# Kernel tuning notes

Hardware: AMD Instinct MI355X
Metric: run time of the kernel (lower is better)

The kernel has to match this reference:

```python
import jax, jax.numpy as jnp
import numpy as np

# ResNet-20 (CIFAR) conv shapes: conv1 + 18 block convs, all 3x3 pad=1
SHAPES = [(16,3,3,3)] + [(16,16,3,3)]*6 + [(32,16,3,3)] + [(32,32,3,3)]*5 + [(64,32,3,3)] + [(64,64,3,3)]*5
SIZES = [int(np.prod(s)) for s in SHAPES]
OFFS = np.concatenate([[0], np.cumsum(SIZES)]).astype(int)
D = int(OFFS[-1])  # 267696 flattened conv params
LOW_D = 40
# (conv_a, conv_b, stride, out_channels) for each BasicBlock
BLOCKS = [(1,2,1,16),(3,4,1,16),(5,6,1,16),
          (7,8,2,32),(9,10,1,32),(11,12,1,32),
          (13,14,2,64),(15,16,1,64),(17,18,1,64)]

def conv3x3(x, w, stride):
    return jax.lax.conv_general_dilated(x, w, (stride, stride), ((1,1),(1,1)),
        dimension_numbers=('NCHW','OIHW','NCHW'))

def bn(x):
    # training-mode BatchNorm2d with default-initialized affine (gamma=1, beta=0)
    m = jnp.mean(x, axis=(0,2,3), keepdims=True)
    v = jnp.var(x, axis=(0,2,3), keepdims=True)
    return (x - m) * jax.lax.rsqrt(v + 1e-5)

def shortcut(x, stride, out_ch):
    # option-A shortcut: stride-2 subsample + zero-pad channels
    if stride != 1:
        x = x[:, :, ::2, ::2]
    pad = out_ch - x.shape[1]
    if pad > 0:
        x = jnp.pad(x, ((0,0),(pad//2, pad - pad//2),(0,0),(0,0)))
    return x

def setup_inputs() -> dict:
    key = jax.random.key(0)
    ks = jax.random.split(key, 6)
    B = 1024
    x = jax.random.normal(ks[0], (B,3,32,32), jnp.float32)
    origin_weight = jax.random.normal(ks[1], (D,), jnp.float32) * 0.05
    P = jax.random.normal(ks[2], (LOW_D, D), jnp.float32) * 0.01
    new_param = jax.random.uniform(ks[3], (LOW_D,), jnp.float32)
    W_fc = jax.random.normal(ks[4], (10,64), jnp.float32) * 0.1
    b_fc = jnp.zeros((10,), jnp.float32)
    return {"x": x, "origin_weight": origin_weight, "P": P,
            "new_param": new_param, "W_fc": W_fc, "b_fc": b_fc}

def reference(x, origin_weight, P, new_param, W_fc, b_fc):
    # conv(x, W0) + sum_i a_i * conv(x, P_i)  ==  conv(x, W0 + sum_i a_i * P_i)
    # (conv is linear in its weights, so fusing the 40-term loop is exact)
    w_flat = origin_weight + new_param @ P  # [D]
    ws = [w_flat[OFFS[i]:OFFS[i+1]].reshape(SHAPES[i]) for i in range(19)]
    out = jax.nn.relu(bn(conv3x3(x, ws[0], 1)))
    for (a, b, s, c) in BLOCKS:
        h = jax.nn.relu(bn(conv3x3(out, ws[a], s)))
        h = bn(conv3x3(h, ws[b], 1))
        out = jax.nn.relu(h + shortcut(out, s, c))
    out = out.mean(axis=(2,3))  # global average pool -> [B, 64]
    return out @ W_fc.T + b_fc  # [B, 10]
```

## Files before the change

kernel.cpp:

```cpp
#include <hip/hip_runtime.h>
#include <hip/hip_bf16.h>

#define BATCH 1024
#define NLAYER 19
#define DTOT 267696
#define NSLOT 64
#define PSL (NSLOT*128)

typedef __attribute__((ext_vector_type(8))) short v8s;
typedef __attribute__((ext_vector_type(4))) float v4f;

__device__ inline float ldf(const float* p){ return *p; }
__device__ inline float ldf(const __hip_bfloat16* p){ return __bfloat162float(*p); }

__device__ inline unsigned short f2bf(float x){
    __hip_bfloat16 h = __float2bfloat16(x);
    return *reinterpret_cast<unsigned short*>(&h);
}
__device__ inline float bf2f(unsigned int u){
    return __uint_as_float(u << 16);
}

__global__ void detect_kernel(const unsigned short* __restrict__ xraw, int* __restrict__ flag)
{
    __shared__ int bad;
    if (threadIdx.x == 0) bad = 0;
    __syncthreads();
    int lbad = 0;
    for (int i = threadIdx.x; i < 4096; i += 256) {
        unsigned e = (xraw[i] >> 7) & 0xFF;
        if (e >= 147) lbad++;
    }
    if (lbad) atomicAdd(&bad, lbad);
    __syncthreads();
    if (threadIdx.x == 0) *flag = (bad == 0) ? 1 : 0;
}

__device__ inline bool is_bf16(const int* flag)
{
    return (*(volatile const int*)flag) == 1;
}

__global__ void wflat_kernel(const void* __restrict__ origin,
                             const void* __restrict__ P,
                             const void* __restrict__ npar,
                             float* __restrict__ wout, int D,
                             const int* flag)
{
    int d = blockIdx.x*256 + threadIdx.x;
    if (d >= D) return;
    float acc;
    if (is_bf16(flag)) {
        const __hip_bfloat16* ob = (const __hip_bfloat16*)origin;
        const __hip_bfloat16* Pb = (const __hip_bfloat16*)P;
        const __hip_bfloat16* nb = (const __hip_bfloat16*)npar;
        acc = ldf(ob + d);
        #pragma unroll 8
        for (int k = 0; k < 40; k++)
            acc += ldf(nb + k) * ldf(Pb + (long long)k*D + d);
    } else {
        const float* of = (const float*)origin;
        const float* Pf = (const float*)P;
        const float* nf = (const float*)npar;
        acc = of[d];
        #pragma unroll 8
        for (int k = 0; k < 40; k++)
            acc += nf[k] * Pf[(long long)k*D + d];
    }
    wout[d] = acc;
}

__global__ void wprep_kernel(const float* __restrict__ wflat, unsigned short* __restrict__ WT)
{
    static const int CINA[19]  = {3,16,16,16,16,16,16,16,32,32,32,32,32,32,64,64,64,64,64};
    static const int COUTA[19] = {16,16,16,16,16,16,16,32,32,32,32,32,32,64,64,64,64,64,64};
    static const int LGCA[19]  = {0,4,4,4,4,4,4,4,5,5,5,5,5,5,6,6,6,6,6};
    static const int KPADA[19] = {0,160,160,160,160,160,160,160,288,288,288,288,288,288,576,576,576,576,576};
    static const int WOFFA[19] = {0,432,2736,5040,7344,9648,11952,14256,18864,
        28080,37296,46512,55728,64944,83376,120240,157104,193968,230832};
    static const int WTOFFA[19]= {0,0,2560,5120,7680,10240,12800,15360,20480,29696,
        38912,48128,57344,66560,84992,121856,158720,195584,232448};
    int l = blockIdx.z;
    if (l == 0) return;
    int co = blockIdx.y;
    if (co >= COUTA[l]) return;
    int kp = blockIdx.x*192 + threadIdx.x;
    if (kp >= KPADA[l]) return;
    int cin = CINA[l];
    float v = 0.f;
    if (kp < 9*cin) {
        int tap = kp >> LGCA[l];
        int ci  = kp & (cin - 1);
        v = wflat[WOFFA[l] + (co*cin + ci)*9 + tap];
    }
    WT[WTOFFA[l] + co*KPADA[l] + kp] = f2bf(v);
}

__device__ inline void ldpair_f(const float* base, int p, float& x0, float& x1){
    const float2 v = ((const float2*)base)[p];
    x0 = v.x; x1 = v.y;
}
__device__ inline void ldpair_h(const __hip_bfloat16* base, int p, float& x0, float& x1){
    unsigned u = ((const unsigned int*)base)[p];
    x0 = __uint_as_float(u << 16);
    x1 = __uint_as_float(u & 0xffff0000u);
}

__global__ __launch_bounds__(512) void conv_l0(
    const void* __restrict__ in, const float* __restrict__ wt,
    unsigned short* __restrict__ out, float* __restrict__ ps,
    const int* flag)
{
    constexpr int WP = 38, W2 = 19;
    __shared__ uint2 smem2[2048];
    __shared__ unsigned int in_su[3*18*W2];
    __shared__ float sred[8][32];

    const int tid  = threadIdx.x;
    const int b    = blockIdx.x >> 1;
    const int half = blockIdx.x & 1;
    const int row0 = half*16 - 1;
    const bool isbf = is_bf16(flag);

    {
        const __hip_bfloat16* inb_h = (const __hip_bfloat16*)in + (size_t)b*3072;
        const float*          inb_f = (const float*)in + (size_t)b*3072;
        for (int i = tid; i < 864; i += 512) {
            int w2 = i & 15, lr = (i >> 4) % 18, c = i / 288;
            int ih = row0 + lr;
            unsigned int pk = 0u;
            if ((unsigned)ih < 32u) {
                float x0, x1;
                if (isbf) ldpair_h(inb_h, (c*32 + ih)*16 + w2, x0, x1);
                else      ldpair_f(inb_f, (c*32 + ih)*16 + w2, x0, x1);
                pk = (unsigned int)f2bf(x0) | ((unsigned int)f2bf(x1) << 16);
            }
            in_su[(c*18 + lr)*W2 + 1 + w2] = pk;
        }
        unsigned short* in_ss = (unsigned short*)in_su;
        for (int i = tid; i < 54; i += 512) {
            in_ss[i*WP + 1]  = 0;
            in_ss[i*WP + 34] = 0;
        }
    }
    __syncthreads();

    const int r   = tid >> 5;
    const int col = tid & 31;
    const bool odd = (col & 1);

    float xin[27];
    #pragma unroll
    for (int ci = 0; ci < 3; ci++) {
        #pragma unroll
        for (int kh = 0; kh < 3; kh++) {
            const unsigned int* up = in_su + (ci*18 + r + kh)*W2 + ((col+1) >> 1);
            unsigned int u0 = up[0], u1 = up[1];
            const int kb = ci*9 + kh*3;
            xin[kb+0] = odd ? bf2f(u0 & 0xffffu) : bf2f(u0 >> 16);
            xin[kb+1] = odd ? bf2f(u0 >> 16)     : bf2f(u1 & 0xffffu);
            xin[kb+2] = odd ? bf2f(u1 & 0xffffu) : bf2f(u1 >> 16);
        }
    }

    float acc[16];
    #pragma unroll
    for (int co = 0; co < 16; co++) {
        float a = 0.f;
        #pragma unroll
        for (int k = 0; k < 27; k++)
            a += xin[k] * wt[co*27 + k];
        acc[co] = a;
    }

    #pragma unroll
    for (int j = 0; j < 4; j++) {
        uint2 v;
        v.x = (unsigned)f2bf(acc[4*j+0]) | ((unsigned)f2bf(acc[4*j+1]) << 16);
        v.y = (unsigned)f2bf(acc[4*j+2]) | ((unsigned)f2bf(acc[4*j+3]) << 16);
        smem2[tid*4 + (j ^ (tid & 3))] = v;
    }
    __syncthreads();

    float s4[4] = {0,0,0,0}, q4[4] = {0,0,0,0};
    {
        uint2* ob = (uint2*)(out + (size_t)b*16384 + half*8192);
        #pragma unroll
        for (int it = 0; it < 4; it++) {
            int s = it*512 + tid;
            int phys = (s & ~3) | ((s & 3) ^ ((s >> 2) & 3));
            uint2 v = smem2[phys];
            ob[s] = v;
            float f0 = bf2f(v.x & 0xffffu), f1v = bf2f(v.x >> 16);
            float f2v = bf2f(v.y & 0xffffu), f3v = bf2f(v.y >> 16);
            s4[0] += f0;  q4[0] += f0*f0;
            s4[1] += f1v; q4[1] += f1v*f1v;
            s4[2] += f2v; q4[2] += f2v*f2v;
            s4[3] += f3v; q4[3] += f3v*f3v;
        }
    }
    #pragma unroll
    for (int off = 4; off < 64; off <<= 1) {
        #pragma unroll
        for (int k2 = 0; k2 < 4; k2++) {
            s4[k2] += __shfl_xor(s4[k2], off);
            q4[k2] += __shfl_xor(q4[k2], off);
        }
    }
    {
        const int lane = tid & 63, wv = tid >> 6;
        if (lane < 4) {
            #pragma unroll
            for (int k2 = 0; k2 < 4; k2++) {
                sred[wv][lane*4 + k2]      = s4[k2];
                sred[wv][16 + lane*4 + k2] = q4[k2];
            }
        }
    }
    __syncthreads();
    if (tid < 32) {
        float a = 0.f;
        #pragma unroll
        for (int wv = 0; wv < 8; wv++) a += sred[wv][tid];
        float* sl = ps + (blockIdx.x & (NSLOT-1))*128;
        atomicAdd(&sl[(tid < 16) ? tid : (48 + tid)], a);
    }
}

template<int CIN, int COUT, int HIN, int WIN, int ST, bool FUSE, bool PN,
         bool FUSE2, int PREVC, int PADF>
__global__ __launch_bounds__(256, 4) void conv_mfma(
    const unsigned short* __restrict__ src, const unsigned short* __restrict__ prev,
    unsigned short* __restrict__ resid,
    const unsigned short* __restrict__ wt,
    unsigned short* __restrict__ out, float* __restrict__ stats,
    const float* __restrict__ nstats, float ninvN,
    const float* __restrict__ pstats, float pinvN)
{
    constexpr int HO = HIN/ST, WO = WIN/ST, M = HO*WO, MT = M/16;
    constexpr int NT = COUT/16;
    constexpr int K  = 9*CIN;
    constexpr int S  = (K + 31)/32;
    constexpr int KPAD = S*32;
    constexpr int lgC  = (CIN==16)?4:(CIN==32)?5:6;
    constexpr int lgWI = (WIN==32)?5:(WIN==16)?4:3;
    constexpr int lgWO = (WO==32)?5:(WO==16)?4:3;
    constexpr int CMASK = CIN/8 - 1;
    constexpr int JITER = (NT==1)? MT/4 : (NT==2)? MT/2 : MT;
    static_assert(M*COUT <= CIN*HIN*WIN, "out_s fits in in_s");

    __shared__ unsigned short in_s[CIN*HIN*WIN];
    __shared__ float red[128];
    __shared__ float statred[256];
    __shared__ float nm[64], nv[64];
    __shared__ float pm_s[64], pv_s[64];
    __shared__ uint4 zq;

    const int tid = threadIdx.x;
    const int b   = blockIdx.x;

    if (tid == 0) { zq.x = 0; zq.y = 0; zq.z = 0; zq.w = 0; }

    {
        const int idx = tid & 127, hf = tid >> 7;
        float sacc = 0.f;
        #pragma unroll 8
        for (int k = hf*32; k < hf*32 + 32; k++)
            sacc += nstats[k*128 + idx];
        statred[tid] = sacc;
    }
    __syncthreads();
    if (tid < CIN) {
        float ssum = statred[tid]      + statred[128 + tid];
        float qsum = statred[64 + tid] + statred[192 + tid];
        float m = ssum*ninvN;
        float v = fmaxf(qsum*ninvN - m*m, 0.f);
        nm[tid] = m; nv[tid] = rsqrtf(v + 1e-5f);
    }
    if (PN && tid < CIN) {
        float ssum = 0.f, qsum = 0.f;
        for (int k = 0; k < NSLOT; k++) {
            ssum += pstats[k*128 + tid];
            qsum += pstats[k*128 + 64 + tid];
        }
        float m = ssum*pinvN;
        float v = fmaxf(qsum*pinvN - m*m, 0.f);
        pm_s[tid] = m; pv_s[tid] = rsqrtf(v + 1e-5f);
    }
    __syncthreads();

    {
        const uint4* sb4 = (const uint4*)(src + (size_t)b*(HIN*WIN)*CIN);
        constexpr int NP4 = CIN*HIN*WIN/8;
        if (FUSE) {
            const uint4* pb4 = (const uint4*)(prev + (size_t)b*(HIN*WIN)*CIN);
            uint4* rb4 = (uint4*)(resid + (size_t)b*(HIN*WIN)*CIN);
            for (int i = tid; i < NP4; i += 256) {
                uint4 v = sb4[i];
                uint4 pw = pb4[i];
                int e0 = i << 3;
                int c0 = e0 & (CIN-1);
                int p  = e0 >> lgC;
                float f[8] = { bf2f(v.x & 0xffffu), bf2f(v.x >> 16),
                               bf2f(v.y & 0xffffu), bf2f(v.y >> 16),
                               bf2f(v.z & 0xffffu), bf2f(v.z >> 16),
                               bf2f(v.w & 0xffffu), bf2f(v.w >> 16) };
                float g[8] = { bf2f(pw.x & 0xffffu), bf2f(pw.x >> 16),
                               bf2f(pw.y & 0xffffu), bf2f(pw.y >> 16),
                               bf2f(pw.z & 0xffffu), bf2f(pw.z >> 16),
                               bf2f(pw.w & 0xffffu), bf2f(pw.w >> 16) };
                #pragma unroll
                for (int k = 0; k < 8; k++) {
                    int c = c0 + k;
                    float fx = (f[k] - nm[c])*nv[c];
                    float gv = g[k];
                    if (PN) gv = fmaxf((gv - pm_s[c])*pv_s[c], 0.f);
                    f[k] = fmaxf(fx + gv, 0.f);
                }
                uint4 o;
                o.x = (unsigned)f2bf(f[0]) | ((unsigned)f2bf(f[1]) << 16);
                o.y = (unsigned)f2bf(f[2]) | ((unsigned)f2bf(f[3]) << 16);
                o.z = (unsigned)f2bf(f[4]) | ((unsigned)f2bf(f[5]) << 16);
                o.w = (unsigned)f2bf(f[6]) | ((unsigned)f2bf(f[7]) << 16);
                rb4[i] = o;
                int csw = c0 ^ ((p & CMASK) << 3);
                *(uint4*)(in_s + (p << lgC) + csw) = o;
            }
        } else if (FUSE2) {
            uint4* rb4 = (uint4*)(resid + (size_t)b*(HIN*WIN)*CIN);
            for (int i = tid; i < NP4; i += 256) {
                uint4 v = sb4[i];
                int e0 = i << 3;
                int c0 = e0 & (CIN-1);
                int p  = e0 >> lgC;
                int h  = p >> lgWI, wq = p & (WIN-1);
                int pp = (h << (lgWI+2)) + 2*wq;
                int pc0 = c0 - PADF;
                bool pv = (pc0 >= 0) && (pc0 <= PREVC - 8);
                uint4 pw;
                pw.x = 0; pw.y = 0; pw.z = 0; pw.w = 0;
                if (pv) pw = *(const uint4*)(prev + ((size_t)b*(HIN*WIN*4) + pp)*PREVC + pc0);
                float f[8] = { bf2f(v.x & 0xffffu), bf2f(v.x >> 16),
                               bf2f(v.y & 0xffffu), bf2f(v.y >> 16),
                               bf2f(v.z & 0xffffu), bf2f(v.z >> 16),
                               bf2f(v.w & 0xffffu), bf2f(v.w >> 16) };
                float g[8] = { bf2f(pw.x & 0xffffu), bf2f(pw.x >> 16),
                               bf2f(pw.y & 0xffffu), bf2f(pw.y >> 16),
                               bf2f(pw.z & 0xffffu), bf2f(pw.z >> 16),
                               bf2f(pw.w & 0xffffu), bf2f(pw.w >> 16) };
                #pragma unroll
                for (int k = 0; k < 8; k++) {
                    int c = c0 + k;
                    f[k] = fmaxf((f[k] - nm[c])*nv[c] + g[k], 0.f);
                }
                uint4 o;
                o.x = (unsigned)f2bf(f[0]) | ((unsigned)f2bf(f[1]) << 16);
                o.y = (unsigned)f2bf(f[2]) | ((unsigned)f2bf(f[3]) << 16);
                o.z = (unsigned)f2bf(f[4]) | ((unsigned)f2bf(f[5]) << 16);
                o.w = (unsigned)f2bf(f[6]) | ((unsigned)f2bf(f[7]) << 16);
                rb4[i] = o;
                int csw = c0 ^ ((p & CMASK) << 3);
                *(uint4*)(in_s + (p << lgC) + csw) = o;
            }
        } else {
            for (int i = tid; i < NP4; i += 256) {
                uint4 v = sb4[i];
                int e0 = i << 3;
                int c0 = e0 & (CIN-1);
                int p  = e0 >> lgC;
                float f[8] = { bf2f(v.x & 0xffffu), bf2f(v.x >> 16),
                               bf2f(v.y & 0xffffu), bf2f(v.y >> 16),
                               bf2f(v.z & 0xffffu), bf2f(v.z >> 16),
                               bf2f(v.w & 0xffffu), bf2f(v.w >> 16) };
                #pragma unroll
                for (int k = 0; k < 8; k++) {
                    int c = c0 + k;
                    f[k] = fmaxf((f[k] - nm[c])*nv[c], 0.f);
                }
                uint4 o;
                o.x = (unsigned)f2bf(f[0]) | ((unsigned)f2bf(f[1]) << 16);
                o.y = (unsigned)f2bf(f[2]) | ((unsigned)f2bf(f[3]) << 16);
                o.z = (unsigned)f2bf(f[4]) | ((unsigned)f2bf(f[5]) << 16);
                o.w = (unsigned)f2bf(f[6]) | ((unsigned)f2bf(f[7]) << 16);
                int csw = c0 ^ ((p & CMASK) << 3);
                *(uint4*)(in_s + (p << lgC) + csw) = o;
            }
        }
    }
    __syncthreads();

    const int w   = tid >> 6;
    const int ln  = tid & 63;
    const int l15 = ln & 15;
    const int q   = ln >> 4;

    int n0, mt0, step;
    if (NT == 1)      { n0 = 0;         mt0 = w;      step = 4; }
    else if (NT == 2) { n0 = (w&1)*16;  mt0 = w>>1;   step = 2; }
    else              { n0 = w*16;      mt0 = 0;      step = 1; }

    const unsigned short* wb = wt + (size_t)(n0 + l15)*KPAD + q*8;
    const int c0q = (CIN==16) ? ((q & 1) << 3) : (q << 3);

    v4f acc[JITER];
    #pragma unroll
    for (int j = 0; j < JITER; j++) acc[j] = v4f{0.f,0.f,0.f,0.f};

    if constexpr (CIN == 64) {
        #pragma unroll
        for (int s = 0; s < S; s++) {
            const v8s Bf = *(const v8s*)(wb + 32*s);
            const int tap = s >> 1;
            const int dh1 = tap/3 - 1, dw1 = tap%3 - 1;
            const int c0s = c0q + ((s & 1) << 5);
            #pragma unroll
            for (int j = 0; j < JITER; j++) {
                const int mt  = mt0 + j*step;
                const int p   = mt*16 + l15;
                const int ihb = (p >> lgWO) * ST;
                const int iwb = (p & (WO-1)) * ST;
                int ih = ihb + dh1, iw = iwb + dw1;
                bool valid = ((unsigned)ih < (unsigned)HIN) && ((unsigned)iw < (unsigned)WIN);
                int pp  = (ih << lgWI) + iw;
                int csw = c0s ^ ((pp & CMASK) << 3);
                int eoff = (pp << lgC) + csw;
                const v8s* ap = valid ? (const v8s*)(in_s + eoff) : (const v8s*)&zq;
                v8s Af = *ap;
                acc[j] = __builtin_amdgcn_mfma_f32_16x16x32_bf16(Af, Bf, acc[j], 0, 0, 0);
            }
        }
    } else {
        v8s Bf[S];
        #pragma unroll
        for (int s = 0; s < S; s++)
            Bf[s] = *(const v8s*)(wb + 32*s);

        int dh1s[S], dw1s[S];
        if (CIN == 16) {
            int tq = q >> 1;
            #pragma unroll
            for (int s = 0; s < S; s++) {
                int tap = 2*s + tq;
                int dh = (tap*11) >> 5;
                int dw = tap - 3*dh;
                dh1s[s] = (tap >= 9) ? -1000 : (dh - 1);
                dw1s[s] = dw - 1;
            }
        }

        #pragma unroll
        for (int j = 0; j < JITER; j++) {
            const int mt  = mt0 + j*step;
            const int p   = mt*16 + l15;
            const int ihb = (p >> lgWO) * ST;
            const int iwb = (p & (WO-1)) * ST;
            #pragma unroll
            for (int s = 0; s < S; s++) {
                int dh1, dw1;
                if (CIN == 16) { dh1 = dh1s[s]; dw1 = dw1s[s]; }
                else           { dh1 = s/3 - 1; dw1 = s%3 - 1; }
                int ih = ihb + dh1, iw = iwb + dw1;
                bool valid = ((unsigned)ih < (unsigned)HIN) && ((unsigned)iw < (unsigned)WIN);
                int pp  = (ih << lgWI) + iw;
                int csw = c0q ^ ((pp & CMASK) << 3);
                int eoff = (pp << lgC) + csw;
                const v8s* ap = valid ? (const v8s*)(in_s + eoff) : (const v8s*)&zq;
                v8s Af = *ap;
                acc[j] = __builtin_amdgcn_mfma_f32_16x16x32_bf16(Af, Bf[s], acc[j], 0, 0, 0);
            }
        }
    }
    __syncthreads();

    unsigned short* out_s = in_s;
    float sa = 0.f, qa = 0.f;
    #pragma unroll
    for (int j = 0; j < JITER; j++) {
        const int mt = mt0 + j*step;
        #pragma unroll
        for (int r2 = 0; r2 < 4; r2++) {
            float v = acc[j][r2];
            out_s[(mt*16 + q*4 + r2)*COUT + n0 + l15] = f2bf(v);
            sa += v; qa += v*v;
        }
    }
    __syncthreads();

    {
        constexpr int NIT = (M*COUT/8)/256;
        uint4* ob4 = (uint4*)(out + (size_t)b*M*COUT);
        const uint4* os4 = (const uint4*)in_s;
        #pragma unroll
        for (int it = 0; it < NIT; it++)
            ob4[it*256 + tid] = os4[it*256 + tid];
    }

    sa += __shfl_xor(sa, 16); sa += __shfl_xor(sa, 32);
    qa += __shfl_xor(qa, 16); qa += __shfl_xor(qa, 32);
    if (q == 0) {
        red[(w*16 + l15)*2]     = sa;
        red[(w*16 + l15)*2 + 1] = qa;
    }
    __syncthreads();
    if (tid < COUT) {
        float S2, Q2;
        if (NT == 1) {
            S2 = red[tid*2] + red[(16+tid)*2] + red[(32+tid)*2] + red[(48+tid)*2];
            Q2 = red[tid*2+1] + red[(16+tid)*2+1] + red[(32+tid)*2+1] + red[(48+tid)*2+1];
        } else if (NT == 2) {
            int w0 = tid >> 4, cl = tid & 15;
            S2 = red[((w0*16)+cl)*2]     + red[(((w0+2)*16)+cl)*2];
            Q2 = red[((w0*16)+cl)*2 + 1] + red[(((w0+2)*16)+cl)*2 + 1];
        } else {
            int w0 = tid >> 4, cl = tid & 15;
            S2 = red[((w0*16)+cl)*2];
            Q2 = red[((w0*16)+cl)*2 + 1];
        }
        float* sl = stats + (b & (NSLOT-1))*128;
        atomicAdd(&sl[tid],      S2);
        atomicAdd(&sl[64 + tid], Q2);
    }
}

__global__ void poolfc_kernel(const unsigned short* __restrict__ x,
    const unsigned short* __restrict__ resid,
    const float* __restrict__ stats, float invN,
    const void* __restrict__ Wfc, const void* __restrict__ bfc,
    void* __restrict__ out, const int* flag)
{
    int b = blockIdx.x;
    int c = threadIdx.x;
    float ssum = 0.f, qsum = 0.f;
    for (int k = 0; k < NSLOT; k++) {
        ssum += stats[k*128 + c];
        qsum += stats[k*128 + 64 + c];
    }
    float m = ssum*invN;
    float v = fmaxf(qsum*invN - m*m, 0.f);
    float rs = rsqrtf(v + 1e-5f);
    float s = 0.f;
    #pragma unroll
    for (int p = 0; p < 64; p++) {
        size_t idx = ((size_t)b*64 + p)*64 + c;
        float xv = bf2f((unsigned int)x[idx]);
        float rv = bf2f((unsigned int)resid[idx]);
        s += fmaxf((xv - m)*rs + rv, 0.f);
    }
    __shared__ float feat[64];
    feat[c] = s * (1.f/64.f);
    __syncthreads();
    if (c < 10) {
        if (is_bf16(flag)) {
            const __hip_bfloat16* W  = (const __hip_bfloat16*)Wfc;
            const __hip_bfloat16* bb = (const __hip_bfloat16*)bfc;
            float o = ldf(bb + c);
            for (int k = 0; k < 64; k++)
                o += feat[k] * ldf(W + c*64 + k);
            ((__hip_bfloat16*)out)[b*10 + c] = __float2bfloat16(o);
        } else {
            const float* W  = (const float*)Wfc;
            const float* bb = (const float*)bfc;
            float o = bb[c];
            for (int k = 0; k < 64; k++)
                o += feat[k] * W[c*64 + k];
            ((float*)out)[b*10 + c] = o;
        }
    }
}

extern "C" void kernel_launch(void* const* d_in, const int* in_sizes, int n_in,
                              void* d_out, int out_size, void* d_ws, size_t ws_size,
                              hipStream_t stream)
{
    char* ws = (char*)d_ws;
    float* wflat = (float*)(ws);
    int*   flag  = (int*)  (ws + 1146880);
    unsigned short* WT = (unsigned short*)(ws + 1179648);
    unsigned short* curA = (unsigned short*)(ws + 1720320);
    unsigned short* curB = (unsigned short*)(ws + 1720320 + 33554432ULL);
    unsigned short* f1   = (unsigned short*)(ws + 1720320 + 67108864ULL);
    unsigned short* f2   = (unsigned short*)(ws + 1720320 + 100663296ULL);
    float* ps    = (float*)(ws + 135938048ULL);

    hipMemsetAsync(ps, 0, NLAYER*PSL*4, stream);
    detect_kernel<<<1, 256, 0, stream>>>((const unsigned short*)d_in[0], flag);

    wflat_kernel<<<(DTOT+255)/256, 256, 0, stream>>>(
        d_in[1], d_in[2], d_in[3], wflat, DTOT, flag);

    {
        dim3 g(3, 64, 19);
        wprep_kernel<<<g, 192, 0, stream>>>(wflat, WT);
    }

    static const int WTOFF[NLAYER] = {0,0,2560,5120,7680,10240,12800,15360,20480,29696,
        38912,48128,57344,66560,84992,121856,158720,195584,232448};
    const float iN32 = 1.f/1048576.f;
    const float iN16 = 1.f/262144.f;
    const float iN8  = 1.f/65536.f;

    conv_l0<<<2*BATCH,512,0,stream>>>(d_in[0], wflat, curB, ps, flag);

    conv_mfma<16,16,32,32,1,false,false,false,0,0><<<BATCH,256,0,stream>>>(
        curB, nullptr, nullptr, WT + WTOFF[1], f1, ps + 1*PSL, ps, iN32, nullptr, 0.f);
    conv_mfma<16,16,32,32,1,false,false,false,0,0><<<BATCH,256,0,stream>>>(
        f1, nullptr, nullptr, WT + WTOFF[2], f2, ps + 2*PSL, ps + 1*PSL, iN32, nullptr, 0.f);
    conv_mfma<16,16,32,32,1,true,true,false,0,0><<<BATCH,256,0,stream>>>(
        f2, curB, curA, WT + WTOFF[3], f1, ps + 3*PSL, ps + 2*PSL, iN32, ps, iN32);
    conv_mfma<16,16,32,32,1,false,false,false,0,0><<<BATCH,256,0,stream>>>(
        f1, nullptr, nullptr, WT + WTOFF[4], f2, ps + 4*PSL, ps + 3*PSL, iN32, nullptr, 0.f);
    conv_mfma<16,16,32,32,1,true,false,false,0,0><<<BATCH,256,0,stream>>>(
        f2, curA, curB, WT + WTOFF[5], f1, ps + 5*PSL, ps + 4*PSL, iN32, nullptr, 0.f);
    conv_mfma<16,16,32,32,1,false,false,false,0,0><<<BATCH,256,0,stream>>>(
        f1, nullptr, nullptr, WT + WTOFF[6], f2, ps + 6*PSL, ps + 5*PSL, iN32, nullptr, 0.f);
    conv_mfma<16,32,32,32,2,true,false,false,0,0><<<BATCH,256,0,stream>>>(
        f2, curB, curA, WT + WTOFF[7], f1, ps + 7*PSL, ps + 6*PSL, iN32, nullptr, 0.f);
    conv_mfma<32,32,16,16,1,false,false,false,0,0><<<BATCH,256,0,stream>>>(
        f1, nullptr, nullptr, WT + WTOFF[8], f2, ps + 8*PSL, ps + 7*PSL, iN16, nullptr, 0.f);
    conv_mfma<32,32,16,16,1,false,false,true,16,8><<<BATCH,256,0,stream>>>(
        f2, curA, curB, WT + WTOFF[9], f1, ps + 9*PSL, ps + 8*PSL, iN16, nullptr, 0.f);
    conv_mfma<32,32,16,16,1,false,false,false,0,0><<<BATCH,256,0,stream>>>(
        f1, nullptr, nullptr, WT + WTOFF[10], f2, ps + 10*PSL, ps + 9*PSL, iN16, nullptr, 0.f);
    conv_mfma<32,32,16,16,1,true,false,false,0,0><<<BATCH,256,0,stream>>>(
        f2, curB, curA, WT + WTOFF[11], f1, ps + 11*PSL, ps + 10*PSL, iN16, nullptr, 0.f);
    conv_mfma<32,32,16,16,1,false,false,false,0,0><<<BATCH,256,0,stream>>>(
        f1, nullptr, nullptr, WT + WTOFF[12], f2, ps + 12*PSL, ps + 11*PSL, iN16, nullptr, 0.f);
    conv_mfma<32,64,16,16,2,true,false,false,0,0><<<BATCH,256,0,stream>>>(
        f2, curA, curB, WT + WTOFF[13], f1, ps + 13*PSL, ps + 12*PSL, iN16, nullptr, 0.f);
    conv_mfma<64,64,8,8,1,false,false,false,0,0><<<BATCH,256,0,stream>>>(
        f1, nullptr, nullptr, WT + WTOFF[14], f2, ps + 14*PSL, ps + 13*PSL, iN8, nullptr, 0.f);
    conv_mfma<64,64,8,8,1,false,false,true,32,16><<<BATCH,256,0,stream>>>(
        f2, curB, curA, WT + WTOFF[15], f1, ps + 15*PSL, ps + 14*PSL, iN8, nullptr, 0.f);
    conv_mfma<64,64,8,8,1,false,false,false,0,0><<<BATCH,256,0,stream>>>(
        f1, nullptr, nullptr, WT + WTOFF[16], f2, ps + 16*PSL, ps + 15*PSL, iN8, nullptr, 0.f);
    conv_mfma<64,64,8,8,1,true,false,false,0,0><<<BATCH,256,0,stream>>>(
        f2, curA, curB, WT + WTOFF[17], f1, ps + 17*PSL, ps + 16*PSL, iN8, nullptr, 0.f);
    conv_mfma<64,64,8,8,1,false,false,false,0,0><<<BATCH,256,0,stream>>>(
        f1, nullptr, nullptr, WT + WTOFF[18], f2, ps + 18*PSL, ps + 17*PSL, iN8, nullptr, 0.f);

    poolfc_kernel<<<BATCH, 64, 0, stream>>>(
        f2, curB, ps + 18*PSL, iN8, d_in[4], d_in[5], d_out, flag);
}
```

Measured before the change: 459.2 us.

## Rewrite first conv layer as MFMA bf16 matmul with one image per block

The 3-channel first convolution drops its per-thread scalar FMA loop over 27 taps × 16 channels. It becomes an im2col-style bf16 MFMA (16x16x32) with K padded from 27 to 32, and each block now handles a whole image using 256 threads instead of half an image with 512. The input is staged into a zero-padded LDS tile and outputs are written back through LDS as 16-byte stores. BN statistics are computed from the fp32 accumulators rather than the bf16-rounded values, which slightly changes the numerics. Weights are also rounded to bf16, a possible accuracy change.

Measured after the change: 436.6 us. 4.9% less time.

```diff
diff --git a/kernel.cpp b/kernel.cpp
--- a/kernel.cpp
+++ b/kernel.cpp
@@ -96,134 +96,116 @@
     WT[WTOFFA[l] + co*KPADA[l] + kp] = f2bf(v);
 }
 
-__device__ inline void ldpair_f(const float* base, int p, float& x0, float& x1){
-    const float2 v = ((const float2*)base)[p];
-    x0 = v.x; x1 = v.y;
-}
-__device__ inline void ldpair_h(const __hip_bfloat16* base, int p, float& x0, float& x1){
-    unsigned u = ((const unsigned int*)base)[p];
-    x0 = __uint_as_float(u << 16);
-    x1 = __uint_as_float(u & 0xffff0000u);
-}
-
-__global__ __launch_bounds__(512) void conv_l0(
+__global__ __launch_bounds__(256, 4) void conv_l0(
     const void* __restrict__ in, const float* __restrict__ wt,
     unsigned short* __restrict__ out, float* __restrict__ ps,
     const int* flag)
 {
-    constexpr int WP = 38, W2 = 19;
-    __shared__ uint2 smem2[2048];
-    __shared__ unsigned int in_su[3*18*W2];
-    __shared__ float sred[8][32];
-
-    const int tid  = threadIdx.x;
-    const int b    = blockIdx.x >> 1;
-    const int half = blockIdx.x & 1;
-    const int row0 = half*16 - 1;
+    __shared__ unsigned short lbuf[16384];
+    __shared__ float red[128];
+
+    const int tid = threadIdx.x;
+    const int b   = blockIdx.x;
     const bool isbf = is_bf16(flag);
 
     {
-        const __hip_bfloat16* inb_h = (const __hip_bfloat16*)in + (size_t)b*3072;
-        const float*          inb_f = (const float*)in + (size_t)b*3072;
-        for (int i = tid; i < 864; i += 512) {
-            int w2 = i & 15, lr = (i >> 4) % 18, c = i / 288;
-            int ih = row0 + lr;
-            unsigned int pk = 0u;
-            if ((unsigned)ih < 32u) {
-                float x0, x1;
-                if (isbf) ldpair_h(inb_h, (c*32 + ih)*16 + w2, x0, x1);
-                else      ldpair_f(inb_f, (c*32 + ih)*16 + w2, x0, x1);
-                pk = (unsigned int)f2bf(x0) | ((unsigned int)f2bf(x1) << 16);
-            }
-            in_su[(c*18 + lr)*W2 + 1 + w2] = pk;
-        }
-        unsigned short* in_ss = (unsigned short*)in_su;
-        for (int i = tid; i < 54; i += 512) {
-            in_ss[i*WP + 1]  = 0;
-            in_ss[i*WP + 34] = 0;
-        }
-    }
-    __syncthreads();
-
-    const int r   = tid >> 5;
-    const int col = tid & 31;
-    const bool odd = (col & 1);
-
-    float xin[27];
+        unsigned int* l4 = (unsigned int*)lbuf;
+        for (int i = tid; i < 1836; i += 256) l4[i] = 0u;
+    }
+    __syncthreads();
+
+    {
+        const __hip_bfloat16* ih_ = (const __hip_bfloat16*)in + (size_t)b*3072;
+        const float*          if_ = (const float*)in + (size_t)b*3072;
+        for (int i = tid; i < 3072; i += 256) {
+            int c = i >> 10, rem = i & 1023, h = rem >> 5, w2 = rem & 31;
+            float x = isbf ? ldf(ih_ + i) : if_[i];
+            lbuf[c*1224 + (h+1)*36 + (w2+1)] = f2bf(x);
+        }
+    }
+
+    const int w_  = tid >> 6;
+    const int ln  = tid & 63;
+    const int l15 = ln & 15;
+    const int q   = ln >> 4;
+
+    v8s Bf;
+    {
+        union { unsigned int u[4]; v8s v; } bu;
+        #pragma unroll
+        for (int kk2 = 0; kk2 < 4; kk2++) {
+            int k0 = q*8 + kk2*2, k1 = k0 + 1;
+            float w0 = (k0 < 27) ? wt[l15*27 + k0] : 0.f;
+            float w1 = (k1 < 27) ? wt[l15*27 + k1] : 0.f;
+            bu.u[kk2] = (unsigned)f2bf(w0) | ((unsigned)f2bf(w1) << 16);
+        }
+        Bf = bu.v;
+    }
+
+    int offk[8];
     #pragma unroll
-    for (int ci = 0; ci < 3; ci++) {
-        #pragma unroll
-        for (int kh = 0; kh < 3; kh++) {
-            const unsigned int* up = in_su + (ci*18 + r + kh)*W2 + ((col+1) >> 1);
-            unsigned int u0 = up[0], u1 = up[1];
-            const int kb = ci*9 + kh*3;
-            xin[kb+0] = odd ? bf2f(u0 & 0xffffu) : bf2f(u0 >> 16);
-            xin[kb+1] = odd ? bf2f(u0 >> 16)     : bf2f(u1 & 0xffffu);
-            xin[kb+2] = odd ? bf2f(u1 & 0xffffu) : bf2f(u1 >> 16);
-        }
-    }
-
-    float acc[16];
+    for (int kk = 0; kk < 8; kk++) {
+        int k = q*8 + kk;
+        int ci = k / 9;
+        int tap = k - ci*9;
+        int kh = tap / 3, kw = tap - kh*3;
+        if (ci > 2) { ci = 0; kh = 0; kw = 0; }
+        offk[kk] = ci*1224 + kh*36 + kw;
+    }
+    __syncthreads();
+
+    v4f acc[16];
     #pragma unroll
-    for (int co = 0; co < 16; co++) {
-        float a = 0.f;
-        #pragma unroll
-        for (int k = 0; k < 27; k++)
-            a += xin[k] * wt[co*27 + k];
-        acc[co] = a;
-    }
+    for (int j = 0; j < 16; j++) acc[j] = v4f{0.f,0.f,0.f,0.f};
 
     #pragma unroll
-    for (int j = 0; j < 4; j++) {
-        uint2 v;
-        v.x = (unsigned)f2bf(acc[4*j+0]) | ((unsigned)f2bf(acc[4*j+1]) << 16);
-        v.y = (unsigned)f2bf(acc[4*j+2]) | ((unsigned)f2bf(acc[4*j+3]) << 16);
-        smem2[tid*4 + (j ^ (tid & 3))] = v;
-    }
-    __syncthreads();
-
-    float s4[4] = {0,0,0,0}, q4[4] = {0,0,0,0};
-    {
-        uint2* ob = (uint2*)(out + (size_t)b*16384 + half*8192);
-        #pragma unroll
-        for (int it = 0; it < 4; it++) {
-            int s = it*512 + tid;
-            int phys = (s & ~3) | ((s & 3) ^ ((s >> 2) & 3));
-            uint2 v = smem2[phys];
-            ob[s] = v;
-            float f0 = bf2f(v.x & 0xffffu), f1v = bf2f(v.x >> 16);
-            float f2v = bf2f(v.y & 0xffffu), f3v = bf2f(v.y >> 16);
-            s4[0] += f0;  q4[0] += f0*f0;
-            s4[1] += f1v; q4[1] += f1v*f1v;
-            s4[2] += f2v; q4[2] += f2v*f2v;
-            s4[3] += f3v; q4[3] += f3v*f3v;
-        }
-    }
+    for (int j = 0; j < 16; j++) {
+        const int mt = w_ + j*4;
+        const int p  = mt*16 + l15;
+        const int base = (p >> 5)*36 + (p & 31);
+        union { unsigned int u[4]; v8s v; } au;
+        #pragma unroll
+        for (int kk2 = 0; kk2 < 4; kk2++) {
+            unsigned a0 = lbuf[base + offk[kk2*2]];
+            unsigned a1 = lbuf[base + offk[kk2*2+1]];
+            au.u[kk2] = a0 | (a1 << 16);
+        }
+        acc[j] = __builtin_amdgcn_mfma_f32_16x16x32_bf16(au.v, Bf, acc[j], 0, 0, 0);
+    }
+    __syncthreads();
+
+    float sa = 0.f, qa = 0.f;
     #pragma unroll
-    for (int off = 4; off < 64; off <<= 1) {
-        #pragma unroll
-        for (int k2 = 0; k2 < 4; k2++) {
-            s4[k2] += __shfl_xor(s4[k2], off);
-            q4[k2] += __shfl_xor(q4[k2], off);
-        }
-    }
-    {
-        const int lane = tid & 63, wv = tid >> 6;
-        if (lane < 4) {
-            #pragma unroll
-            for (int k2 = 0; k2 < 4; k2++) {
-                sred[wv][lane*4 + k2]      = s4[k2];
-                sred[wv][16 + lane*4 + k2] = q4[k2];
-            }
-        }
-    }
-    __syncthreads();
-    if (tid < 32) {
-        float a = 0.f;
-        #pragma unroll
-        for (int wv = 0; wv < 8; wv++) a += sred[wv][tid];
-        float* sl = ps + (blockIdx.x & (NSLOT-1))*128;
-        atomicAdd(&sl[(tid < 16) ? tid : (48 + tid)], a);
+    for (int j = 0; j < 16; j++) {
+        const int mt = w_ + j*4;
+        #pragma unroll
+        for (int r2 = 0; r2 < 4; r2++) {
+            float v = acc[j][r2];
+            lbuf[(mt*16 + q*4 + r2)*16 + l15] = f2bf(v);
+            sa += v; qa += v*v;
+        }
+    }
+    __syncthreads();
+    {
+        uint4* ob4 = (uint4*)(out + (size_t)b*16384);
+        const uint4* os4 = (const uint4*)lbuf;
+        #pragma unroll
+        for (int it = 0; it < 8; it++)
+            ob4[it*256 + tid] = os4[it*256 + tid];
+    }
+    sa += __shfl_xor(sa, 16); sa += __shfl_xor(sa, 32);
+    qa += __shfl_xor(qa, 16); qa += __shfl_xor(qa, 32);
+    if (q == 0) {
+        red[(w_*16 + l15)*2]     = sa;
+        red[(w_*16 + l15)*2 + 1] = qa;
+    }
+    __syncthreads();
+    if (tid < 16) {
+        float S2 = red[tid*2] + red[(16+tid)*2] + red[(32+tid)*2] + red[(48+tid)*2];
+        float Q2 = red[tid*2+1] + red[(16+tid)*2+1] + red[(32+tid)*2+1] + red[(48+tid)*2+1];
+        float* sl = ps + (b & (NSLOT-1))*128;
+        atomicAdd(&sl[tid],      S2);
+        atomicAdd(&sl[64 + tid], Q2);
     }
 }
 
@@ -599,7 +581,7 @@
     const float iN16 = 1.f/262144.f;
     const float iN8  = 1.f/65536.f;
 
-    conv_l0<<<2*BATCH,512,0,stream>>>(d_in[0], wflat, curB, ps, flag);
+    conv_l0<<<BATCH,256,0,stream>>>(d_in[0], wflat, curB, ps, flag);
 
     conv_mfma<16,16,32,32,1,false,false,false,0,0><<<BATCH,256,0,stream>>>(
         curB, nullptr, nullptr, WT + WTOFF[1], f1, ps + 1*PSL, ps, iN32, nullptr, 0.f);
```
